# Kernel tuning notes

Measured on AMD Instinct MI355X. Metric: run time of the kernel, lower is better.

The kernel has to match this reference:

```python
import jax, jax.numpy as jnp
import numpy as np

N = 4096
FEAT = 64


def _pairwise_dist(x):
    # x: [N, F] -> symmetric [N, N] Euclidean distance matrix, zero diagonal
    sq = jnp.sum(x * x, axis=-1)
    d2 = sq[:, None] + sq[None, :] - 2.0 * (x @ x.T)
    d = jnp.sqrt(jnp.maximum(d2, 0.0))
    return d * (1.0 - jnp.eye(x.shape[0], dtype=x.dtype))


def setup_inputs() -> dict:
    key = jax.random.key(0)
    k1, k2 = jax.random.split(key)
    x1 = jax.random.normal(k1, (N, FEAT), dtype=jnp.float32)
    x2 = jax.random.normal(k2, (N, FEAT), dtype=jnp.float32)
    return {"d1": _pairwise_dist(x1), "d2": _pairwise_dist(x2)}


def _mst_edges(d):
    # Prim's algorithm, O(N^2). For a distance matrix with generic (distinct)
    # entries the MST is unique and its N-1 edges are exactly the 0-dim
    # persistence pairs returned by the union-find PersistentHomologyCalculation.
    n = d.shape[0]
    INF = jnp.asarray(jnp.finfo(d.dtype).max, d.dtype)
    in_tree = jnp.zeros((n,), dtype=bool).at[0].set(True)
    min_dist = d[0]                       # best edge weight into the tree per node
    parent = jnp.zeros((n,), dtype=jnp.int32)  # tree endpoint of that best edge

    def step(carry, _):
        in_tree, min_dist, parent = carry
        masked = jnp.where(in_tree, INF, min_dist)
        j = jnp.argmin(masked).astype(jnp.int32)
        edge = jnp.stack([parent[j], j])  # (tree node, new node)
        in_tree = in_tree.at[j].set(True)
        dj = d[j]
        upd = (dj < min_dist) & (~in_tree)
        min_dist = jnp.where(upd, dj, min_dist)
        parent = jnp.where(upd, j, parent)
        return (in_tree, min_dist, parent), edge

    _, edges = jax.lax.scan(step, (in_tree, min_dist, parent), None, length=n - 1)
    return edges  # [N-1, 2] int32; d is symmetric so pair order is irrelevant


def reference(d1, d2):
    # Pairings are computed on detached CPU copies in the original -> no grad
    p1 = _mst_edges(jax.lax.stop_gradient(d1))
    p2 = jax.lax.stop_gradient(_mst_edges(jax.lax.stop_gradient(d2)))
    sig1 = d1[p1[:, 0], p1[:, 1]]
    sig2 = d2[p2[:, 0], p2[:, 1]]
    # match_edges == 'symmetric'
    sig1_2 = d2[p1[:, 0], p1[:, 1]]
    sig2_1 = d1[p2[:, 0], p2[:, 1]]
    return jnp.sum((sig1 - sig1_2) ** 2) + jnp.sum((sig2 - sig2_1) ** 2)
```

## Files before the change

### kernel.cpp

```cpp
#include <hip/hip_runtime.h>
#include <stdint.h>


#define N        4096
#define NROUNDS  12

typedef unsigned long long u64;
typedef uint32_t u32;

struct Ws {
    u64 best[2][N];
    u32 comp[2][N];
    u32 edges[2][N];
    u32 ncomp[2];
};

__device__ __forceinline__ u64 shfl_down_u64(u64 x, int off) {
    u32 lo = (u32)x, hi = (u32)(x >> 32);
    lo = (u32)__shfl_down((int)lo, off, 64);
    hi = (u32)__shfl_down((int)hi, off, 64);
    return ((u64)hi << 32) | lo;
}

__global__ void init_k(Ws* __restrict__ ws) {
    int i = blockIdx.x * blockDim.x + threadIdx.x;
    if (i < N) {
        ws->best[0][i] = ~0ull; ws->best[1][i] = ~0ull;
        ws->comp[0][i] = (u32)i; ws->comp[1][i] = (u32)i;
        u32 diag = ((u32)i << 12) | (u32)i;
        ws->edges[0][i] = diag; ws->edges[1][i] = diag;
        if (i < 2) ws->ncomp[i] = (u32)N;
    }
}

__launch_bounds__(256, 8)
__global__ void scan_k(const float* __restrict__ d1, const float* __restrict__ d2,
                       Ws* __restrict__ ws, int first) {
    const int m = blockIdx.x >> 10;
    if (ws->ncomp[m] <= 1u) return;
    const int wave = threadIdx.x >> 6, lane = threadIdx.x & 63;
    const int v = ((blockIdx.x & 1023) << 2) + wave;

    const float* __restrict__ dm = m ? d2 : d1;
    const u32*   __restrict__ cm = ws->comp[m];
    const float4* __restrict__ row4 = (const float4*)(dm + (size_t)v * N);
    const uint4*  __restrict__ c4   = (const uint4*)cm;
    const u32 cv = first ? (u32)v : cm[v];

    float wmin = __int_as_float(0x7F800000);
    u32   colmin = 0u;

    #pragma unroll
    for (int bb = 0; bb < 4; ++bb) {
        float4 w[4];
        uint4  cu[4];
        #pragma unroll
        for (int i = 0; i < 4; ++i) {
            const int c = lane + 64 * (bb * 4 + i);
            w[i] = row4[c];
            if (!first) cu[i] = c4[c];
        }
        #pragma unroll
        for (int i = 0; i < 4; ++i) {
            const u32 c0 = (u32)(4 * (lane + 64 * (bb * 4 + i)));
            if (first) {
                const u32 uv = (u32)v;
                if (c0+0 != uv && w[i].x < wmin) { wmin = w[i].x; colmin = c0+0; }
                if (c0+1 != uv && w[i].y < wmin) { wmin = w[i].y; colmin = c0+1; }
                if (c0+2 != uv && w[i].z < wmin) { wmin = w[i].z; colmin = c0+2; }
                if (c0+3 != uv && w[i].w < wmin) { wmin = w[i].w; colmin = c0+3; }
            } else {
                if (cu[i].x != cv && w[i].x < wmin) { wmin = w[i].x; colmin = c0+0; }
                if (cu[i].y != cv && w[i].y < wmin) { wmin = w[i].y; colmin = c0+1; }
                if (cu[i].z != cv && w[i].z < wmin) { wmin = w[i].z; colmin = c0+2; }
                if (cu[i].w != cv && w[i].w < wmin) { wmin = w[i].w; colmin = c0+3; }
            }
        }
    }

    u64 kmin = ((u64)__float_as_uint(wmin) << 32) | (u64)colmin;
    #pragma unroll
    for (int off = 32; off >= 1; off >>= 1) {
        u64 o = shfl_down_u64(kmin, off);
        if (o < kmin) kmin = o;
    }
    if (lane == 0) {
        u32 wb = (u32)(kmin >> 32);
        u32 u  = (u32)kmin & 0xFFFu;
        u32 lo = min((u32)v, u), hi = max((u32)v, u);
        u64 g  = ((u64)wb << 24) | ((u64)lo << 12) | (u64)hi;
        if (first) {
            ws->best[m][v] = g;
        } else {
            if (g < ws->best[m][cv])
                atomicMin(&ws->best[m][cv], g);
        }
    }
}

__launch_bounds__(1024, 1)
__global__ void hook_k(Ws* __restrict__ ws) {
    const int m = blockIdx.x;
    const int tid = threadIdx.x;
    if (ws->ncomp[m] <= 1u) return;

    u32* __restrict__ gcomp = ws->comp[m];
    u64* __restrict__ best  = ws->best[m];

    __shared__ u32 compL[N];
    __shared__ u32 nxtA[N];
    __shared__ u32 nxtB[N];
    __shared__ u32 red[16];

    {
        uint4* dst = (uint4*)compL;
        const uint4* src = (const uint4*)gcomp;
        if (tid < N / 4) dst[tid] = src[tid];
    }
    __syncthreads();

    bool isroot[4];
    u64  bkey[4];

    #pragma unroll
    for (int k = 0; k < 4; ++k) {
        int i = tid + k * 1024;
        u32 x = (u32)i;
        bool r = (compL[i] == (u32)i);
        isroot[k] = r;
        u64 g = 0;
        if (r) {
            g = best[i];
            u32 lo = (u32)(g >> 12) & 0xFFFu;
            u32 hi = (u32)g & 0xFFFu;
            u32 cl = compL[lo], ch = compL[hi];
            x = (cl == (u32)i) ? ch : cl;
        }
        bkey[k] = g;
        nxtA[i] = x;
    }
    __syncthreads();

    #pragma unroll
    for (int k = 0; k < 4; ++k) {
        int i = tid + k * 1024;
        u32 nn = (u32)i;
        if (isroot[k]) {
            u32 o = nxtA[i];
            bool mutual = (nxtA[o] == (u32)i);
            nn = (mutual && ((u32)i < o)) ? (u32)i : o;
            if (nn != (u32)i)
                ws->edges[m][i] = (u32)(bkey[k] & 0xFFFFFFu);
        }
        nxtB[i] = nn;
    }
    __syncthreads();

    for (int s = 0; s < 12; ++s) {
        #pragma unroll
        for (int k = 0; k < 4; ++k) {
            int i = tid + k * 1024;
            nxtB[i] = nxtB[nxtB[i]];
        }
        __syncthreads();
    }

    u32 cnt = 0;
    #pragma unroll
    for (int k = 0; k < 4; ++k) {
        int i = tid + k * 1024;
        if (isroot[k] && nxtB[i] == (u32)i) cnt++;
    }
    #pragma unroll
    for (int off = 32; off >= 1; off >>= 1) cnt += (u32)__shfl_down((int)cnt, off, 64);
    const int lane = tid & 63, wave = tid >> 6;
    if (lane == 0) red[wave] = cnt;
    __syncthreads();

    #pragma unroll
    for (int k = 0; k < 4; ++k) {
        int i = tid + k * 1024;
        gcomp[i] = nxtB[compL[i]];
        if (isroot[k]) best[i] = ~0ull;
    }
    if (tid == 0) {
        u32 t = 0;
        #pragma unroll
        for (int w = 0; w < 16; ++w) t += red[w];
        ws->ncomp[m] = t;
    }
}

__launch_bounds__(256, 1)
__global__ void epi_k(const float* __restrict__ d1, const float* __restrict__ d2,
                      Ws* __restrict__ ws, float* __restrict__ out) {
    const int m = blockIdx.x, tid = threadIdx.x;
    float acc = 0.f;
    for (int i = tid; i < N; i += 256) {
        u32 pk = ws->edges[m][i];
        u32 lo = (pk >> 12) & 0xFFFu, hi = pk & 0xFFFu;
        size_t off = (size_t)lo * N + hi;
        float df = d1[off] - d2[off];
        acc += df * df;
    }
    #pragma unroll
    for (int off = 32; off >= 1; off >>= 1) acc += __shfl_down(acc, off, 64);
    __shared__ float part[4];
    const int lane = tid & 63, wave = tid >> 6;
    if (lane == 0) part[wave] = acc;
    __syncthreads();
    if (tid == 0) atomicAdd(out, part[0] + part[1] + part[2] + part[3]);
}

extern "C" void kernel_launch(void* const* d_in, const int* in_sizes, int n_in,
                              void* d_out, int out_size, void* d_ws, size_t ws_size,
                              hipStream_t stream) {
    (void)in_sizes; (void)n_in; (void)out_size; (void)ws_size;
    const float* d1 = (const float*)d_in[0];
    const float* d2 = (const float*)d_in[1];
    float* out = (float*)d_out;
    Ws* ws = (Ws*)d_ws;

    hipMemsetAsync(d_out, 0, sizeof(float), stream);
    init_k<<<dim3(16), dim3(256), 0, stream>>>(ws);
    for (int r = 0; r < NROUNDS; ++r) {
        scan_k<<<dim3(2048), dim3(256), 0, stream>>>(d1, d2, ws, r == 0 ? 1 : 0);
        hook_k<<<dim3(2), dim3(1024), 0, stream>>>(ws);
    }
    epi_k<<<dim3(2), dim3(256), 0, stream>>>(d1, d2, ws, out);
}
```

Before: 314.9 us.

## Cache per-bucket row minima to skip rescanning distance rows in Boruvka rounds

In the first round each row is split into 64 buckets of 64 columns, and the minimum key of every bucket is stored in a new 4 MB workspace array. Later rounds first look up each bucket's cached minimum and check whether it still crosses a component boundary. A bucket is rescanned only when its cached minimum now lies inside the row's own component and is smaller than the best cross-component candidate, so far less of the 2x64 MB of matrix data is read in later rounds. The cost is extra workspace, a 64-bit key layout with shuffle reductions, and a fallback to the old full scan when the workspace is too small.

```diff
diff --git a/kernel.cpp b/kernel.cpp
--- a/kernel.cpp
+++ b/kernel.cpp
@@ -7,13 +7,19 @@
 
 typedef unsigned long long u64;
 typedef uint32_t u32;
+
+#define INFK (~0ull)
 
 struct Ws {
     u64 best[2][N];
     u32 comp[2][N];
     u32 edges[2][N];
     u32 ncomp[2];
+    u32 pad[14];
+    u64 bm[2][N * 64];
 };
+
+__device__ __forceinline__ u64 umin64(u64 a, u64 b) { return a < b ? a : b; }
 
 __device__ __forceinline__ u64 shfl_down_u64(u64 x, int off) {
     u32 lo = (u32)x, hi = (u32)(x >> 32);
@@ -21,11 +27,17 @@
     hi = (u32)__shfl_down((int)hi, off, 64);
     return ((u64)hi << 32) | lo;
 }
+__device__ __forceinline__ u64 shfl_xor_u64(u64 x, int off) {
+    u32 lo = (u32)x, hi = (u32)(x >> 32);
+    lo = (u32)__shfl_xor((int)lo, off, 64);
+    hi = (u32)__shfl_xor((int)hi, off, 64);
+    return ((u64)hi << 32) | lo;
+}
 
 __global__ void init_k(Ws* __restrict__ ws) {
     int i = blockIdx.x * blockDim.x + threadIdx.x;
     if (i < N) {
-        ws->best[0][i] = ~0ull; ws->best[1][i] = ~0ull;
+        ws->best[0][i] = INFK; ws->best[1][i] = INFK;
         ws->comp[0][i] = (u32)i; ws->comp[1][i] = (u32)i;
         u32 diag = ((u32)i << 12) | (u32)i;
         ws->edges[0][i] = diag; ws->edges[1][i] = diag;
@@ -34,26 +46,121 @@
 }
 
 __launch_bounds__(256, 8)
-__global__ void scan_k(const float* __restrict__ d1, const float* __restrict__ d2,
-                       Ws* __restrict__ ws, int first) {
+__global__ void scanA_k(const float* __restrict__ d1, const float* __restrict__ d2,
+                        Ws* __restrict__ ws) {
+    const int m = blockIdx.x >> 10;
+    const int wave = threadIdx.x >> 6, lane = threadIdx.x & 63;
+    const int v = ((blockIdx.x & 1023) << 2) + wave;
+    const float4* __restrict__ row4 = (const float4*)((m ? d2 : d1) + (size_t)v * N);
+    u64* __restrict__ bmrow = ws->bm[m] + (size_t)v * 64;
+
+    __shared__ u64 bs[4][64];
+
+    const u32 uv = (u32)v;
+    u64 rowmin = INFK;
+
+    #pragma unroll
+    for (int i = 0; i < 16; ++i) {
+        const int c = lane + 64 * i;
+        float4 w = row4[c];
+        const u32 c0 = (u32)(4 * c);
+        u64 k0 = (c0 + 0 == uv) ? INFK : ((((u64)__float_as_uint(w.x)) << 12) | (c0 + 0));
+        u64 k1 = (c0 + 1 == uv) ? INFK : ((((u64)__float_as_uint(w.y)) << 12) | (c0 + 1));
+        u64 k2 = (c0 + 2 == uv) ? INFK : ((((u64)__float_as_uint(w.z)) << 12) | (c0 + 2));
+        u64 k3 = (c0 + 3 == uv) ? INFK : ((((u64)__float_as_uint(w.w)) << 12) | (c0 + 3));
+        u64 kk = umin64(umin64(k0, k1), umin64(k2, k3));
+        #pragma unroll
+        for (int off = 1; off <= 8; off <<= 1)
+            kk = umin64(kk, shfl_xor_u64(kk, off));
+        if ((lane & 15) == 0) bs[wave][4 * i + (lane >> 4)] = kk;
+        rowmin = umin64(rowmin, kk);
+    }
+    rowmin = umin64(rowmin, shfl_xor_u64(rowmin, 16));
+    rowmin = umin64(rowmin, shfl_xor_u64(rowmin, 32));
+
+    __syncthreads();
+    bmrow[lane] = bs[wave][lane];
+
+    if (lane == 0) {
+        u32 wb = (u32)(rowmin >> 12);
+        u32 u  = (u32)rowmin & 0xFFFu;
+        u32 lo = min(uv, u), hi = max(uv, u);
+        ws->best[m][v] = ((u64)wb << 24) | ((u64)lo << 12) | (u64)hi;
+    }
+}
+
+__launch_bounds__(256, 8)
+__global__ void scan2_k(const float* __restrict__ d1, const float* __restrict__ d2,
+                        Ws* __restrict__ ws) {
     const int m = blockIdx.x >> 10;
     if (ws->ncomp[m] <= 1u) return;
     const int wave = threadIdx.x >> 6, lane = threadIdx.x & 63;
     const int v = ((blockIdx.x & 1023) << 2) + wave;
 
+    const float* __restrict__ dm = m ? d2 : d1;
+    const u32*   __restrict__ cm = ws->comp[m];
+    u64* __restrict__ bmrow = ws->bm[m] + (size_t)v * 64;
+
+    const u32 cv = cm[v];
+    u64 key = bmrow[lane];
+    bool cross = false;
+    if (key != INFK) cross = (cm[(u32)key & 0xFFFu] != cv);
+
+    u64 kb = cross ? key : INFK;
+    #pragma unroll
+    for (int off = 1; off <= 32; off <<= 1)
+        kb = umin64(kb, shfl_xor_u64(kb, off));
+
+    const bool need = (!cross) && (key < kb);
+    u64 nm = INFK;
+    if (need) {
+        const float4* __restrict__ row4 = (const float4*)(dm + (size_t)v * N);
+        const uint4*  __restrict__ c4   = (const uint4*)cm;
+        #pragma unroll
+        for (int j = 0; j < 16; ++j) {
+            float4 w = row4[lane * 16 + j];
+            uint4 cu = c4[lane * 16 + j];
+            u32 c0 = (u32)(4 * (lane * 16 + j));
+            if (cu.x != cv) nm = umin64(nm, (((u64)__float_as_uint(w.x)) << 12) | (c0 + 0));
+            if (cu.y != cv) nm = umin64(nm, (((u64)__float_as_uint(w.y)) << 12) | (c0 + 1));
+            if (cu.z != cv) nm = umin64(nm, (((u64)__float_as_uint(w.z)) << 12) | (c0 + 2));
+            if (cu.w != cv) nm = umin64(nm, (((u64)__float_as_uint(w.w)) << 12) | (c0 + 3));
+        }
+        bmrow[lane] = nm;
+    }
+    u64 kb2 = need ? nm : INFK;
+    #pragma unroll
+    for (int off = 1; off <= 32; off <<= 1)
+        kb2 = umin64(kb2, shfl_xor_u64(kb2, off));
+
+    u64 fin = umin64(kb, kb2);
+    if (lane == 0 && fin != INFK) {
+        u32 wb = (u32)(fin >> 12);
+        u32 u  = (u32)fin & 0xFFFu;
+        u32 lo = min((u32)v, u), hi = max((u32)v, u);
+        u64 g  = ((u64)wb << 24) | ((u64)lo << 12) | (u64)hi;
+        if (g < ws->best[m][cv])
+            atomicMin(&ws->best[m][cv], g);
+    }
+}
+
+__launch_bounds__(256, 8)
+__global__ void scanF_k(const float* __restrict__ d1, const float* __restrict__ d2,
+                        Ws* __restrict__ ws, int first) {
+    const int m = blockIdx.x >> 10;
+    if (ws->ncomp[m] <= 1u) return;
+    const int wave = threadIdx.x >> 6, lane = threadIdx.x & 63;
+    const int v = ((blockIdx.x & 1023) << 2) + wave;
     const float* __restrict__ dm = m ? d2 : d1;
     const u32*   __restrict__ cm = ws->comp[m];
     const float4* __restrict__ row4 = (const float4*)(dm + (size_t)v * N);
     const uint4*  __restrict__ c4   = (const uint4*)cm;
     const u32 cv = first ? (u32)v : cm[v];
-
     float wmin = __int_as_float(0x7F800000);
-    u32   colmin = 0u;
-
+    u32 colmin = 0u;
     #pragma unroll
     for (int bb = 0; bb < 4; ++bb) {
-        float4 w[4];
-        uint4  cu[4];
+        float4 w[4]; uint4 cu[4];
         #pragma unroll
         for (int i = 0; i < 4; ++i) {
             const int c = lane + 64 * (bb * 4 + i);
@@ -77,24 +184,17 @@
             }
         }
     }
-
     u64 kmin = ((u64)__float_as_uint(wmin) << 32) | (u64)colmin;
     #pragma unroll
-    for (int off = 32; off >= 1; off >>= 1) {
-        u64 o = shfl_down_u64(kmin, off);
-        if (o < kmin) kmin = o;
-    }
+    for (int off = 32; off >= 1; off >>= 1)
+        kmin = umin64(kmin, shfl_down_u64(kmin, off));
     if (lane == 0) {
         u32 wb = (u32)(kmin >> 32);
         u32 u  = (u32)kmin & 0xFFFu;
         u32 lo = min((u32)v, u), hi = max((u32)v, u);
         u64 g  = ((u64)wb << 24) | ((u64)lo << 12) | (u64)hi;
-        if (first) {
-            ws->best[m][v] = g;
-        } else {
-            if (g < ws->best[m][cv])
-                atomicMin(&ws->best[m][cv], g);
-        }
+        if (first) ws->best[m][v] = g;
+        else if (g < ws->best[m][cv]) atomicMin(&ws->best[m][cv], g);
     }
 }
 
@@ -181,7 +281,7 @@
     for (int k = 0; k < 4; ++k) {
         int i = tid + k * 1024;
         gcomp[i] = nxtB[compL[i]];
-        if (isroot[k]) best[i] = ~0ull;
+        if (isroot[k]) best[i] = INFK;
     }
     if (tid == 0) {
         u32 t = 0;
@@ -215,16 +315,22 @@
 extern "C" void kernel_launch(void* const* d_in, const int* in_sizes, int n_in,
                               void* d_out, int out_size, void* d_ws, size_t ws_size,
                               hipStream_t stream) {
-    (void)in_sizes; (void)n_in; (void)out_size; (void)ws_size;
+    (void)in_sizes; (void)n_in; (void)out_size;
     const float* d1 = (const float*)d_in[0];
     const float* d2 = (const float*)d_in[1];
     float* out = (float*)d_out;
     Ws* ws = (Ws*)d_ws;
+    const bool big = (ws_size >= sizeof(Ws));
 
     hipMemsetAsync(d_out, 0, sizeof(float), stream);
     init_k<<<dim3(16), dim3(256), 0, stream>>>(ws);
     for (int r = 0; r < NROUNDS; ++r) {
-        scan_k<<<dim3(2048), dim3(256), 0, stream>>>(d1, d2, ws, r == 0 ? 1 : 0);
+        if (big) {
+            if (r == 0) scanA_k<<<dim3(2048), dim3(256), 0, stream>>>(d1, d2, ws);
+            else        scan2_k<<<dim3(2048), dim3(256), 0, stream>>>(d1, d2, ws);
+        } else {
+            scanF_k<<<dim3(2048), dim3(256), 0, stream>>>(d1, d2, ws, r == 0 ? 1 : 0);
+        }
         hook_k<<<dim3(2), dim3(1024), 0, stream>>>(ws);
     }
     epi_k<<<dim3(2), dim3(256), 0, stream>>>(d1, d2, ws, out);
```

Measured after the change: 281.0 us. 10.8% less time.
